# Performance work log

Measured on AMD Instinct MI355X. Metric: run time of the kernel, lower is better.

## Reference

```python
import jax, jax.numpy as jnp
import numpy as np

MODES1 = [8, 8, 12, 12]
MODES2 = [8, 8, 12, 12]
MODES3 = [8, 8, 8, 8]
LAYERS = [20, 24, 24, 32, 32]
FC_DIM = 128
IN_DIM = 5
OUT_DIM = 3
B, GX, GY, GT = 4, 128, 128, 20


def _gelu(v):
    # torch F.gelu default is the exact (erf) variant
    return jax.nn.gelu(v, approximate=False)


def _spectral_conv(x, w, m1, m2, m3):
    """x: (B,Ci,X,Y,T) float; w: (4,2,Ci,Co,m1,m2,m3) float (real/imag stacked)."""
    wc = w[:, 0] + 1j * w[:, 1]  # (4,Ci,Co,m1,m2,m3) complex64
    bs, _, X, Y, T = x.shape
    Co = wc.shape[2]
    x_ft = jnp.fft.rfftn(x, axes=(2, 3, 4))  # (B,Ci,X,Y,T//2+1) complex
    zd = min(x_ft.shape[4], m3)

    def corner(xs, ys):
        c = x_ft[:, :, xs, ys, :zd]
        # zero-pad z axis up to m3 (mirrors the zero-initialized `coeff` buffer)
        return jnp.pad(c, [(0, 0)] * 4 + [(0, m3 - zd)])

    lo1, hi1 = slice(0, m1), slice(X - m1, X)
    lo2, hi2 = slice(0, m2), slice(Y - m2, Y)
    o1 = jnp.einsum('bixyz,ioxyz->boxyz', corner(lo1, lo2), wc[0])
    o2 = jnp.einsum('bixyz,ioxyz->boxyz', corner(hi1, lo2), wc[1])
    o3 = jnp.einsum('bixyz,ioxyz->boxyz', corner(lo1, hi2), wc[2])
    o4 = jnp.einsum('bixyz,ioxyz->boxyz', corner(hi1, hi2), wc[3])

    out_ft = jnp.zeros((bs, Co, X, Y, m3), dtype=x_ft.dtype)
    out_ft = out_ft.at[:, :, :m1, :m2].set(o1)
    out_ft = out_ft.at[:, :, X - m1:, :m2].set(o2)
    out_ft = out_ft.at[:, :, :m1, Y - m2:].set(o3)
    out_ft = out_ft.at[:, :, X - m1:, Y - m2:].set(o4)
    # irfftn with s=(X,Y,T) zero-pads the truncated z axis back up, like torch
    return jnp.fft.irfftn(out_ft, s=(X, Y, T), axes=(2, 3, 4))


def setup_inputs() -> dict:
    key = jax.random.key(0)
    ks = iter(jax.random.split(key, 64))
    inp = {}
    inp['x'] = jax.random.normal(next(ks), (B, GX, GY, GT, IN_DIM), dtype=jnp.float32)
    inp['fc0_w'] = jax.random.normal(next(ks), (IN_DIM, LAYERS[0]), dtype=jnp.float32) * 0.1
    inp['fc0_b'] = jnp.zeros((LAYERS[0],), dtype=jnp.float32)
    for i in range(4):
        ci, co = LAYERS[i], LAYERS[i + 1]
        scale = 1.0 / (ci * co)
        inp[f's{i}_w'] = jax.random.uniform(
            next(ks), (4, 2, ci, co, MODES1[i], MODES2[i], MODES3[i]), dtype=jnp.float32) * scale
        inp[f'c{i}_w'] = jax.random.normal(next(ks), (co, ci), dtype=jnp.float32) * (1.0 / np.sqrt(ci))
        inp[f'c{i}_b'] = jnp.zeros((co,), dtype=jnp.float32)
    inp['fc1_w'] = jax.random.normal(next(ks), (LAYERS[-1], FC_DIM), dtype=jnp.float32) * (1.0 / np.sqrt(LAYERS[-1]))
    inp['fc1_b'] = jnp.zeros((FC_DIM,), dtype=jnp.float32)
    inp['fc2_w'] = jax.random.normal(next(ks), (FC_DIM, OUT_DIM), dtype=jnp.float32) * (1.0 / np.sqrt(FC_DIM))
    inp['fc2_b'] = jnp.zeros((OUT_DIM,), dtype=jnp.float32)
    return inp


def reference(x, fc0_w, fc0_b,
              s0_w, c0_w, c0_b,
              s1_w, c1_w, c1_b,
              s2_w, c2_w, c2_b,
              s3_w, c3_w, c3_b,
              fc1_w, fc1_b, fc2_w, fc2_b):
    h = x @ fc0_w + fc0_b                       # (B,X,Y,T,C0)
    h = jnp.transpose(h, (0, 4, 1, 2, 3))       # (B,C0,X,Y,T)
    sws = [s0_w, s1_w, s2_w, s3_w]
    cws = [c0_w, c1_w, c2_w, c3_w]
    cbs = [c0_b, c1_b, c2_b, c3_b]
    for i in range(4):
        x1 = _spectral_conv(h, sws[i], MODES1[i], MODES2[i], MODES3[i])
        x2 = jnp.einsum('bixyz,oi->boxyz', h, cws[i]) + cbs[i][None, :, None, None, None]
        h = x1 + x2
        if i != 3:
            h = _gelu(h)
    h = jnp.transpose(h, (0, 2, 3, 4, 1))       # (B,X,Y,T,C_last)
    h = _gelu(h @ fc1_w + fc1_b)
    return h @ fc2_w + fc2_b                    # (B,X,Y,T,out_dim)
```

## Files before the change

kernel.cpp:

```cpp
#include <hip/hip_runtime.h>

#define TWO_PI 6.2831853071795864769f
#define SP3 327680
#define YT 2560

static constexpr float TWC20[20]={
  1.0f, 0.9510565163f, 0.8090169944f, 0.5877852523f, 0.3090169944f,
  0.0f,-0.3090169944f,-0.5877852523f,-0.8090169944f,-0.9510565163f,
 -1.0f,-0.9510565163f,-0.8090169944f,-0.5877852523f,-0.3090169944f,
  0.0f, 0.3090169944f, 0.5877852523f, 0.8090169944f, 0.9510565163f};
static constexpr float TWS20[20]={
  0.0f, 0.3090169944f, 0.5877852523f, 0.8090169944f, 0.9510565163f,
  1.0f, 0.9510565163f, 0.8090169944f, 0.5877852523f, 0.3090169944f,
  0.0f,-0.3090169944f,-0.5877852523f,-0.8090169944f,-0.9510565163f,
 -1.0f,-0.9510565163f,-0.8090169944f,-0.5877852523f,-0.3090169944f};

static __device__ __forceinline__ float gelu_f(float u){
  float x=u*0.7071067811865475f;
  float a=fabsf(x);
  float t=__builtin_amdgcn_rcpf(fmaf(0.3275911f,a,1.0f));
  float p=fmaf(fmaf(fmaf(fmaf(1.061405429f,t,-1.453152027f),t,1.421413741f),t,
               -0.284496736f),t,0.254829592f)*t;
  float e=__expf(-a*a);
  float er=copysignf(1.0f-p*e,x);
  return 0.5f*u*(1.0f+er);
}

__global__ void k_fc0(const float* __restrict__ x, const float* __restrict__ w,
                      const float* __restrict__ bias, float* __restrict__ h){
  __shared__ float wl[100], bl[20];
  int tid=threadIdx.x;
  if(tid<100) wl[tid]=w[tid];
  if(tid<20) bl[tid]=bias[tid];
  __syncthreads();
  int p=blockIdx.x*256+tid;
  int b=p/SP3, sp=p-b*SP3;
  const float* xp=x+(long)p*5;
  float xi[5];
  #pragma unroll
  for(int i=0;i<5;i++) xi[i]=xp[i];
  float* hb=h+(long)(b*32)*SP3+sp;
  #pragma unroll
  for(int c=0;c<20;c++){
    float a=bl[c];
    #pragma unroll
    for(int i=0;i<5;i++) a+=xi[i]*wl[i*20+c];
    hb[(long)c*SP3]=a;
  }
}

template<int M2>
__global__ __launch_bounds__(512,3) void k_fwd_ty8(const float* __restrict__ h,
                                                   float* __restrict__ Fty, int Ci){
  constexpr int J=2*M2*8;
  __shared__ float2 Gc[128*33];
  __shared__ float2 tw128[128];
  int tid=threadIdx.x;
  int bid=blockIdx.x;
  int xg=bid&15, bc=bid>>4; int c=bc%Ci, b=bc/Ci;
  int x0=xg*8;
  if(tid<128){ float s,cc; sincosf(TWO_PI*tid/128.0f,&s,&cc); tw128[tid]=make_float2(cc,s); }
  __syncthreads();
  const float* hb=h+(long)(b*32+c)*SP3+x0*YT;
  float2* outp=(float2*)Fty+((long)(b*32+c)*128+x0)*J;

  for(int half=0;half<2;half++){
    if(half) __syncthreads();
    {
      int y=tid&127, xl=tid>>7;
      const float* rp=hb+(half*4+xl)*YT+y*20;
      float4 r0=*(const float4*)(rp);
      float4 r1=*(const float4*)(rp+4);
      float4 r2=*(const float4*)(rp+8);
      float4 r3=*(const float4*)(rp+12);
      float4 r4=*(const float4*)(rp+16);
      float row[20]={r0.x,r0.y,r0.z,r0.w, r1.x,r1.y,r1.z,r1.w, r2.x,r2.y,r2.z,r2.w,
                     r3.x,r3.y,r3.z,r3.w, r4.x,r4.y,r4.z,r4.w};
      float av[10],bv[10];
      #pragma unroll
      for(int t=0;t<10;t++){av[t]=row[t]+row[t+10]; bv[t]=row[t]-row[t+10];}
      float re[8],im[8];
      #pragma unroll
      for(int kz=0;kz<8;kz++){re[kz]=0.f;im[kz]=0.f;}
      #pragma unroll
      for(int t=0;t<10;t++){
        #pragma unroll
        for(int kz=0;kz<8;kz++){
          float v=(kz&1)?bv[t]:av[t];
          re[kz]+=v*TWC20[(kz*t)%20];
          im[kz]-=v*TWS20[(kz*t)%20];
        }
      }
      #pragma unroll
      for(int kz=0;kz<8;kz++) Gc[y*33+xl*8+kz]=make_float2(re[kz],im[kz]);
    }
    __syncthreads();
    for(int pi=tid;pi<2048;pi+=512){
      int y=pi>>5, col=pi&31;
      float2 a=Gc[y*33+col], bb=Gc[(y+64)*33+col];
      Gc[y*33+col]      =make_float2(a.x+bb.x, a.y+bb.y);
      Gc[(y+64)*33+col] =make_float2(a.x-bb.x, a.y-bb.y);
    }
    __syncthreads();
    for(int ip=tid;ip<(M2+1)*32;ip+=512){
      int col=ip&31, sp=ip>>5;
      int off=(sp&1)?64:0;
      float a1r=0.f,a1i=0.f,a2r=0.f,a2i=0.f;
      int jj=0;
      for(int y=0;y<64;y++){
        float2 w=tw128[jj];
        float2 d=Gc[(y+off)*33+col];
        float tr=d.x*w.x, ts=d.y*w.y, ur=d.y*w.x, us=d.x*w.y;
        a1r+=tr+ts; a1i+=ur-us;
        a2r+=tr-ts; a2i+=ur+us;
        jj=(jj+sp)&127;
      }
      int xl=col>>3, kz=col&7;
      long rowoff=(long)(half*4+xl)*J;
      if(sp<M2) outp[rowoff+sp*8+kz]=make_float2(a1r,a1i);
      if(sp>=1) outp[rowoff+(2*M2-sp)*8+kz]=make_float2(a2r,a2i);
    }
  }
}

template<int M1,int M2>
__global__ __launch_bounds__(256,3) void k_fwd_x2(const float* __restrict__ Fty,
                                                  float* __restrict__ Fm, int Ci){
  constexpr int J=2*M2*8;
  constexpr int NIT=(M1*J+255)/256;
  __shared__ float2 tile[32*J];
  __shared__ float2 tw128[128];
  int tid=threadIdx.x, bid=blockIdx.x;
  int sh=bid&1; int c=(bid>>1)%Ci; int b=bid/(2*Ci);
  if(tid<128){ float s,cc; sincosf(TWO_PI*tid/128.0f,&s,&cc); tw128[tid]=make_float2(cc,s); }
  float accr[NIT],acci[NIT];
  #pragma unroll
  for(int it=0;it<NIT;it++){accr[it]=0.f;acci[it]=0.f;}
  const float2* base=(const float2*)Fty+((long)(b*32+c)*128)*J;
  for(int xt=0;xt<4;xt++){
    __syncthreads();
    const float2* src=base+(long)xt*32*J;
    for(int idx=tid;idx<32*J;idx+=256) tile[idx]=src[idx];
    __syncthreads();
    #pragma unroll
    for(int it=0;it<NIT;it++){
      int idx=it*256+tid;
      if(idx<M1*J){
        int si=idx/J, j=idx-si*J;
        int km=(sh==0)? si : (si-M1);
        int jj=(km*(xt*32))&127;
        float ar=accr[it], ai=acci[it];
        for(int xl=0;xl<32;xl++){
          float2 w=tw128[jj];
          float2 d=tile[xl*J+j];
          ar+=d.x*w.x+d.y*w.y;
          ai+=d.y*w.x-d.x*w.y;
          jj=(jj+km)&127;
        }
        accr[it]=ar; acci[it]=ai;
      }
    }
  }
  float2* o=(float2*)Fm+(long)(b*32+c)*(2*M1)*J;
  #pragma unroll
  for(int it=0;it<NIT;it++){
    int idx=it*256+tid;
    if(idx<M1*J){
      int si=idx/J, j=idx-si*J;
      int s=sh*M1+si;
      o[(long)s*J+j]=make_float2(accr[it],acci[it]);
    }
  }
}

__global__ void k_mix(const float* __restrict__ Fm, const float* __restrict__ w,
                      float* __restrict__ Fm2, int Ci, int Co, int m1, int m2){
  int MC=m1*m2*8;
  int nch=MC/8;
  int bid=blockIdx.x;
  int chunk=bid%nch; int q=(bid/nch)&3; int b=bid/(4*nch);
  int tid=threadIdx.x;
  int M1S=2*m1, M2S=2*m2;
  int J=M2S*8;
  __shared__ float fin[32*16];
  for(int idx=tid;idx<Ci*16;idx+=blockDim.x){
    int i=idx>>4; int r=idx&15; int mll=r>>1; int ri=r&1;
    int mg=chunk*8+mll;
    int mx=mg/(m2*8); int my=(mg>>3)%m2; int kz=mg&7;
    int sx=(q&1)?(m1+mx):mx; int sy=(q&2)?(m2+my):my;
    fin[idx]=Fm[((long)((b*32+i)*M1S+sx)*J+sy*8+kz)*2+ri];
  }
  __syncthreads();
  int ml=tid&7, o=tid>>3;
  int mg=chunk*8+ml;
  int mx=mg/(m2*8); int my=(mg>>3)%m2; int kz=mg&7;
  int sx=(q&1)?(m1+mx):mx; int sy=(q&2)?(m2+my):my;
  int moff=(mx*m2+my)*8+kz;
  const float* wr=w+(long)(q*2)*Ci*Co*MC+o*MC+moff;
  const float* wi=wr+(long)Ci*Co*MC;
  long wstep=(long)Co*MC;
  float re=0.f, im=0.f;
  for(int i=0;i<Ci;i++){
    float ar=fin[i*16+ml*2], ai=fin[i*16+ml*2+1];
    float wrv=wr[i*wstep], wiv=wi[i*wstep];
    re+=ar*wrv-ai*wiv;
    im+=ar*wiv+ai*wrv;
  }
  long oidx=((long)((b*32+o)*M1S+sx)*J+sy*8+kz)*2;
  Fm2[oidx]=re; Fm2[oidx+1]=im;
}

template<int M>
__global__ __launch_bounds__(512,(M==8)?3:2) void k_inv_ytx8(const float* __restrict__ Fm2,
                                                    float* h, int Co, int do_gelu){
  constexpr int S1=2*M, S2=2*M;
  constexpr int J=S2*8;
  __shared__ __align__(16) float uni[10752];
  __shared__ __align__(16) float2 g1s[S2*66];
  __shared__ float2 tw128[128];
  int tid=threadIdx.x;
  int bid=blockIdx.x;
  int xg=bid&15, bo=bid>>4; int oc=bo%Co, b=bo/Co;
  int x0=xg*8;
  if(tid<128){ float s,cc; sincosf(TWO_PI*tid/128.0f,&s,&cc); tw128[tid]=make_float2(cc,s); }
  float2* Fm2s=(float2*)uni;
  const float2* src=(const float2*)Fm2+(long)(b*32+oc)*S1*J;
  for(int idx=tid;idx<S1*J;idx+=512) Fm2s[idx]=src[idx];
  __syncthreads();
  for(int idx=tid;idx<8*J;idx+=512){
    int xl=idx/J, j=idx-xl*J;
    int xgl=x0+xl;
    float re=0.f, im=0.f;
    int jj=0;
    for(int s=0;s<M;s++){
      float2 w=tw128[jj]; float2 d=Fm2s[s*J+j];
      re+=d.x*w.x-d.y*w.y;
      im+=d.x*w.y+d.y*w.x;
      jj=(jj+xgl)&127;
    }
    jj=((128-M)*xgl)&127;
    for(int s=M;s<S1;s++){
      float2 w=tw128[jj]; float2 d=Fm2s[s*J+j];
      re+=d.x*w.x-d.y*w.y;
      im+=d.x*w.y+d.y*w.x;
      jj=(jj+xgl)&127;
    }
    g1s[(j>>3)*66 + xl*8 + (j&7)]=make_float2(re,im);
  }
  __syncthreads();
  float* So=uni;
  const float invN=1.0f/(128.0f*128.0f*20.0f);
  float* hb=h+(long)(b*32+oc)*SP3+x0*YT;
  const float4* g4c=(const float4*)g1s;
  for(int half=0;half<2;half++){
    int y=tid&127, xlh=tid>>7;
    int xlg=half*4+xlh;
    float gyr[8],gyi[8];
    {
      int base=(xlg*8)>>1;
      #pragma unroll
      for(int q=0;q<4;q++){
        float4 d=g4c[base+q];
        gyr[2*q]=d.x;   gyi[2*q]=d.y;
        gyr[2*q+1]=d.z; gyi[2*q+1]=d.w;
      }
    }
    {
      int jm=((128-M)*y)&127;
      float ang=(float)jm*(TWO_PI/128.0f);
      float wx=__cosf(ang), wy=__sinf(ang);
      int base=(M*66+xlg*8)>>1;
      #pragma unroll
      for(int q=0;q<4;q++){
        float4 d=g4c[base+q];
        gyr[2*q]  +=d.x*wx-d.y*wy;  gyi[2*q]  +=d.x*wy+d.y*wx;
        gyr[2*q+1]+=d.z*wx-d.w*wy;  gyi[2*q+1]+=d.z*wy+d.w*wx;
      }
    }
    for(int s=1;s<M;s++){
      int jm=(s*y)&127;
      float ang=(float)jm*(TWO_PI/128.0f);
      float c=__cosf(ang), sn=__sinf(ang);
      int b1=(s*66+xlg*8)>>1, b2=((S2-s)*66+xlg*8)>>1;
      #pragma unroll
      for(int q=0;q<4;q++){
        float4 d1=g4c[b1+q], d2=g4c[b2+q];
        float Ax=d1.x+d2.x, By=d1.y-d2.y, Bx=d1.x-d2.x, Ay=d1.y+d2.y;
        gyr[2*q]  +=Ax*c-By*sn;  gyi[2*q]  +=Bx*sn+Ay*c;
        float Az=d1.z+d2.z, Bw=d1.w-d2.w, Bz=d1.z-d2.z, Aw=d1.w+d2.w;
        gyr[2*q+1]+=Az*c-Bw*sn;  gyi[2*q+1]+=Bz*sn+Aw*c;
      }
    }
    #pragma unroll
    for(int t=0;t<10;t++){
      float E=gyr[0], O=0.f;
      #pragma unroll
      for(int kz=1;kz<8;kz++){
        float term=2.0f*TWC20[(kz*t)%20]*gyr[kz]-2.0f*TWS20[(kz*t)%20]*gyi[kz];
        if(kz&1) O+=term; else E+=term;
      }
      So[tid*21+t]   =(E+O)*invN;
      So[tid*21+t+10]=(E-O)*invN;
    }
    __syncthreads();
    float* dst=hb+half*10240;
    for(int f=tid;f<10240;f+=512){
      int rr=f/20, t=f-rr*20;
      float u=dst[f]+So[rr*21+t];
      if(do_gelu) u=gelu_f(u);
      dst[f]=u;
    }
    __syncthreads();
  }
}

template<int CO>
__global__ __launch_bounds__(256,4) void k_pconv2(float* h, const float* __restrict__ w,
                                                  const float* __restrict__ bias, int Ci){
  __shared__ __align__(16) float wt[32*CO];
  __shared__ float bl[CO];
  int tid=threadIdx.x;
  for(int idx=tid;idx<Ci*CO;idx+=256){int i=idx/CO,o=idx-i*CO; wt[idx]=w[o*Ci+i];}
  if(tid<CO) bl[tid]=bias[tid];
  __syncthreads();
  long p=(long)blockIdx.x*512+tid*2;
  int b=(int)(p/SP3); int sp=(int)(p-(long)b*SP3);
  float* hb=h+(long)b*32*SP3+sp;
  float acc0[CO],acc1[CO];
  #pragma unroll
  for(int o=0;o<CO;o++){acc0[o]=bl[o];acc1[o]=bl[o];}
  for(int i=0;i<Ci;i++){
    float2 v=*(const float2*)&hb[(long)i*SP3];
    const float4* wc=(const float4*)&wt[i*CO];
    #pragma unroll
    for(int o4=0;o4<CO/4;o4++){
      float4 ww=wc[o4];
      acc0[4*o4+0]+=v.x*ww.x; acc0[4*o4+1]+=v.x*ww.y;
      acc0[4*o4+2]+=v.x*ww.z; acc0[4*o4+3]+=v.x*ww.w;
      acc1[4*o4+0]+=v.y*ww.x; acc1[4*o4+1]+=v.y*ww.y;
      acc1[4*o4+2]+=v.y*ww.z; acc1[4*o4+3]+=v.y*ww.w;
    }
  }
  #pragma unroll
  for(int o=0;o<CO;o++){
    *(float2*)&hb[(long)o*SP3]=make_float2(acc0[o],acc1[o]);
  }
}

__global__ void k_prep_w1t(const float* __restrict__ w1, float* __restrict__ w1t){
  int idx=blockIdx.x*256+threadIdx.x;
  if(idx<4096){ int jj=idx>>5, i=idx&31; w1t[idx]=w1[i*128+jj]; }
}

__global__ __launch_bounds__(256,3) void k_head_s(const float* __restrict__ h,
                       const float* __restrict__ w1t, const float* __restrict__ b1,
                       const float* __restrict__ w2, const float* __restrict__ b2,
                       float* __restrict__ out){
  long p=(long)blockIdx.x*512+threadIdx.x;
  int b=(int)(p/SP3); int sp=(int)(p-(long)b*SP3);
  const float* hb=h+(long)b*32*SP3+sp;
  float hv0[32],hv1[32];
  #pragma unroll
  for(int i=0;i<32;i++){hv0[i]=hb[(long)i*SP3]; hv1[i]=hb[(long)i*SP3+256];}
  float a00=b2[0],a01=b2[1],a02=b2[2];
  float a10=a00,a11=a01,a12=a02;
  for(int jj=0;jj<128;jj++){
    const float* wc=w1t+jj*32;
    float u0=b1[jj], u1=u0;
    #pragma unroll
    for(int q=0;q<32;q++){
      float ww=wc[q];
      u0+=hv0[q]*ww;
      u1+=hv1[q]*ww;
    }
    u0=gelu_f(u0); u1=gelu_f(u1);
    float w20=w2[jj*3], w21=w2[jj*3+1], w22=w2[jj*3+2];
    a00+=u0*w20; a01+=u0*w21; a02+=u0*w22;
    a10+=u1*w20; a11+=u1*w21; a12+=u1*w22;
  }
  float* op=out+p*3;
  op[0]=a00; op[1]=a01; op[2]=a02;
  op=out+(p+256)*3;
  op[0]=a10; op[1]=a11; op[2]=a12;
}

__global__ __launch_bounds__(256,4) void k_head2(const float* __restrict__ h,
                       const float* __restrict__ w1, const float* __restrict__ b1,
                       const float* __restrict__ w2, const float* __restrict__ b2,
                       float* __restrict__ out){
  __shared__ __align__(16) float w1t[128*32];
  __shared__ float b1l[128];
  __shared__ __align__(16) float4 w2l[128];
  __shared__ float b2l[3];
  int tid=threadIdx.x;
  for(int idx=tid;idx<4096;idx+=256){int jj=idx>>5,i=idx&31; w1t[idx]=w1[i*128+jj];}
  if(tid<128){b1l[tid]=b1[tid]; w2l[tid]=make_float4(w2[tid*3],w2[tid*3+1],w2[tid*3+2],0.f);}
  if(tid<3) b2l[tid]=b2[tid];
  __syncthreads();
  long p=(long)blockIdx.x*512+tid;
  int b=(int)(p/SP3); int sp=(int)(p-(long)b*SP3);
  const float* hb=h+(long)b*32*SP3+sp;
  float hv0[32],hv1[32];
  #pragma unroll
  for(int i=0;i<32;i++){hv0[i]=hb[(long)i*SP3]; hv1[i]=hb[(long)i*SP3+256];}
  float a00=b2l[0],a01=b2l[1],a02=b2l[2];
  float a10=a00,a11=a01,a12=a02;
  for(int jj=0;jj<128;jj++){
    const float4* wc=(const float4*)&w1t[jj*32];
    float u0=b1l[jj], u1=u0;
    #pragma unroll
    for(int q=0;q<8;q++){
      float4 ww=wc[q];
      u0+=hv0[4*q]*ww.x+hv0[4*q+1]*ww.y+hv0[4*q+2]*ww.z+hv0[4*q+3]*ww.w;
      u1+=hv1[4*q]*ww.x+hv1[4*q+1]*ww.y+hv1[4*q+2]*ww.z+hv1[4*q+3]*ww.w;
    }
    u0=gelu_f(u0); u1=gelu_f(u1);
    float4 w2v=w2l[jj];
    a00+=u0*w2v.x; a01+=u0*w2v.y; a02+=u0*w2v.z;
    a10+=u1*w2v.x; a11+=u1*w2v.y; a12+=u1*w2v.z;
  }
  float* op=out+p*3;
  op[0]=a00; op[1]=a01; op[2]=a02;
  op=out+(p+256)*3;
  op[0]=a10; op[1]=a11; op[2]=a12;
}

extern "C" void kernel_launch(void* const* d_in, const int* in_sizes, int n_in,
                              void* d_out, int out_size, void* d_ws, size_t ws_size,
                              hipStream_t stream){
  (void)in_sizes; (void)n_in; (void)out_size;
  const float* x    =(const float*)d_in[0];
  const float* fc0w =(const float*)d_in[1];
  const float* fc0b =(const float*)d_in[2];
  const float* sw[4]={(const float*)d_in[3],(const float*)d_in[6],(const float*)d_in[9],(const float*)d_in[12]};
  const float* cw[4]={(const float*)d_in[4],(const float*)d_in[7],(const float*)d_in[10],(const float*)d_in[13]};
  const float* cb[4]={(const float*)d_in[5],(const float*)d_in[8],(const float*)d_in[11],(const float*)d_in[14]};
  const float* fc1w =(const float*)d_in[15];
  const float* fc1b =(const float*)d_in[16];
  const float* fc2w =(const float*)d_in[17];
  const float* fc2b =(const float*)d_in[18];
  float* out=(float*)d_out;
  float* ws=(float*)d_ws;

  const long H_FLOATS   = 41943040L;
  const long FTY_FULL   = 6291456L;
  const long FM_FULL    = 1179648L;
  const long NEED_FULL  = H_FLOATS + FTY_FULL + 2*FM_FULL;

  float* h = ws;
  bool full = (ws_size >= (size_t)NEED_FULL*4);

  const int LAY[5]={20,24,24,32,32};
  const int M1A[4]={8,8,12,12};

  k_fc0<<<5120,256,0,stream>>>(x,fc0w,fc0b,h);

  for(int L=0;L<4;L++){
    int Ci=LAY[L], Co=LAY[L+1], m1=M1A[L], m2=M1A[L];
    int nch=m1*m2;
    long FM_B=(long)32*(2*m1)*(2*m2*8)*2;

    if(full){
      float* Fty=ws+H_FLOATS;
      float* Fm =ws+H_FLOATS+FTY_FULL;
      float* Fm2=ws+H_FLOATS+FTY_FULL+FM_FULL;
      if(m1==8)  k_fwd_ty8<8> <<<4*Ci*16,512,0,stream>>>(h,Fty,Ci);
      else       k_fwd_ty8<12><<<4*Ci*16,512,0,stream>>>(h,Fty,Ci);
      if(m1==8)  k_fwd_x2<8,8>  <<<4*Ci*2,256,0,stream>>>(Fty,Fm,Ci);
      else       k_fwd_x2<12,12><<<4*Ci*2,256,0,stream>>>(Fty,Fm,Ci);
      k_mix<<<4*4*nch,Co*8,0,stream>>>(Fm,sw[L],Fm2,Ci,Co,m1,m2);
      if(Co==24) k_pconv2<24><<<2560,256,0,stream>>>(h,cw[L],cb[L],Ci);
      else       k_pconv2<32><<<2560,256,0,stream>>>(h,cw[L],cb[L],Ci);
      if(m1==8)  k_inv_ytx8<8> <<<4*Co*16,512,0,stream>>>(Fm2,h,Co,(L!=3)?1:0);
      else       k_inv_ytx8<12><<<4*Co*16,512,0,stream>>>(Fm2,h,Co,(L!=3)?1:0);
    } else {
      float* Fty=out;
      float* Fm =out+1572864;
      float* Fm2=out+1867776;
      for(int b=0;b<4;b++){
        float* hbp=h+(long)b*32*SP3;
        if(m1==8)  k_fwd_ty8<8> <<<Ci*16,512,0,stream>>>(hbp,Fty,Ci);
        else       k_fwd_ty8<12><<<Ci*16,512,0,stream>>>(hbp,Fty,Ci);
        if(m1==8)  k_fwd_x2<8,8>  <<<Ci*2,256,0,stream>>>(Fty,Fm,Ci);
        else       k_fwd_x2<12,12><<<Ci*2,256,0,stream>>>(Fty,Fm,Ci);
        k_mix<<<4*nch,Co*8,0,stream>>>(Fm,sw[L],Fm2+b*FM_B,Ci,Co,m1,m2);
      }
      if(Co==24) k_pconv2<24><<<2560,256,0,stream>>>(h,cw[L],cb[L],Ci);
      else       k_pconv2<32><<<2560,256,0,stream>>>(h,cw[L],cb[L],Ci);
      for(int b=0;b<4;b++){
        float* hbp=h+(long)b*32*SP3;
        if(m1==8)  k_inv_ytx8<8> <<<Co*16,512,0,stream>>>(Fm2+b*FM_B,hbp,Co,(L!=3)?1:0);
        else       k_inv_ytx8<12><<<Co*16,512,0,stream>>>(Fm2+b*FM_B,hbp,Co,(L!=3)?1:0);
      }
    }
  }
  if(full){
    float* w1t=ws+H_FLOATS+FTY_FULL;
    k_prep_w1t<<<16,256,0,stream>>>(fc1w,w1t);
    k_head_s<<<2560,256,0,stream>>>(h,w1t,fc1b,fc2w,fc2b,out);
  } else {
    k_head2<<<2560,256,0,stream>>>(h,fc1w,fc1b,fc2w,fc2b,out);
  }
}
```

Baseline: 1.486 ms.

## Restructure inverse spectral kernel with y-parity split and direct float4 writes

The inverse y/t transform kernel now runs 256-thread blocks that each cover 4 x-rows instead of 8, doubling the grid. It splits the y-sum into even and odd frequency parts, so each thread produces outputs for both y and y+64 from one pass of twiddle work. Results go straight into h through float4 read-modify-write, which removes the staging shared buffer, its barriers and the shared-memory copy of Fm2 (now read from global directly). This cuts shared memory and synchronisation and halves the trig work, at the cost of more registers per thread and uncached global reads of Fm2.

```diff
diff --git a/kernel.cpp b/kernel.cpp
--- a/kernel.cpp
+++ b/kernel.cpp
@@ -211,106 +211,118 @@
 }
 
 template<int M>
-__global__ __launch_bounds__(512,(M==8)?3:2) void k_inv_ytx8(const float* __restrict__ Fm2,
+__global__ __launch_bounds__(256,4) void k_inv_ytx8(const float* __restrict__ Fm2g,
                                                     float* h, int Co, int do_gelu){
   constexpr int S1=2*M, S2=2*M;
   constexpr int J=S2*8;
-  __shared__ __align__(16) float uni[10752];
-  __shared__ __align__(16) float2 g1s[S2*66];
+  constexpr int GST=34;
+  __shared__ __align__(16) float2 g1s[S2*GST];
   __shared__ float2 tw128[128];
-  int tid=threadIdx.x;
-  int bid=blockIdx.x;
-  int xg=bid&15, bo=bid>>4; int oc=bo%Co, b=bo/Co;
-  int x0=xg*8;
+  int tid=threadIdx.x, bid=blockIdx.x;
+  int xg=bid&31, bo=bid>>5; int oc=bo%Co, b=bo/Co;
+  int x0=xg*4;
   if(tid<128){ float s,cc; sincosf(TWO_PI*tid/128.0f,&s,&cc); tw128[tid]=make_float2(cc,s); }
-  float2* Fm2s=(float2*)uni;
-  const float2* src=(const float2*)Fm2+(long)(b*32+oc)*S1*J;
-  for(int idx=tid;idx<S1*J;idx+=512) Fm2s[idx]=src[idx];
-  __syncthreads();
-  for(int idx=tid;idx<8*J;idx+=512){
+  __syncthreads();
+  const float2* Fm2=(const float2*)Fm2g+(long)(b*32+oc)*S1*J;
+  for(int idx=tid;idx<4*J;idx+=256){
     int xl=idx/J, j=idx-xl*J;
     int xgl=x0+xl;
     float re=0.f, im=0.f;
     int jj=0;
     for(int s=0;s<M;s++){
-      float2 w=tw128[jj]; float2 d=Fm2s[s*J+j];
-      re+=d.x*w.x-d.y*w.y;
-      im+=d.x*w.y+d.y*w.x;
+      float2 w=tw128[jj]; float2 d=Fm2[s*J+j];
+      re+=d.x*w.x-d.y*w.y; im+=d.x*w.y+d.y*w.x;
       jj=(jj+xgl)&127;
     }
     jj=((128-M)*xgl)&127;
     for(int s=M;s<S1;s++){
-      float2 w=tw128[jj]; float2 d=Fm2s[s*J+j];
-      re+=d.x*w.x-d.y*w.y;
-      im+=d.x*w.y+d.y*w.x;
+      float2 w=tw128[jj]; float2 d=Fm2[s*J+j];
+      re+=d.x*w.x-d.y*w.y; im+=d.x*w.y+d.y*w.x;
       jj=(jj+xgl)&127;
     }
-    g1s[(j>>3)*66 + xl*8 + (j&7)]=make_float2(re,im);
-  }
-  __syncthreads();
-  float* So=uni;
+    g1s[(j>>3)*GST + xl*8 + (j&7)]=make_float2(re,im);
+  }
+  __syncthreads();
   const float invN=1.0f/(128.0f*128.0f*20.0f);
   float* hb=h+(long)(b*32+oc)*SP3+x0*YT;
   const float4* g4c=(const float4*)g1s;
-  for(int half=0;half<2;half++){
-    int y=tid&127, xlh=tid>>7;
-    int xlg=half*4+xlh;
-    float gyr[8],gyi[8];
-    {
-      int base=(xlg*8)>>1;
-      #pragma unroll
-      for(int q=0;q<4;q++){
-        float4 d=g4c[base+q];
-        gyr[2*q]=d.x;   gyi[2*q]=d.y;
-        gyr[2*q+1]=d.z; gyi[2*q+1]=d.w;
-      }
-    }
-    {
-      int jm=((128-M)*y)&127;
-      float ang=(float)jm*(TWO_PI/128.0f);
-      float wx=__cosf(ang), wy=__sinf(ang);
-      int base=(M*66+xlg*8)>>1;
-      #pragma unroll
-      for(int q=0;q<4;q++){
-        float4 d=g4c[base+q];
-        gyr[2*q]  +=d.x*wx-d.y*wy;  gyi[2*q]  +=d.x*wy+d.y*wx;
-        gyr[2*q+1]+=d.z*wx-d.w*wy;  gyi[2*q+1]+=d.z*wy+d.w*wx;
-      }
-    }
-    for(int s=1;s<M;s++){
-      int jm=(s*y)&127;
-      float ang=(float)jm*(TWO_PI/128.0f);
-      float c=__cosf(ang), sn=__sinf(ang);
-      int b1=(s*66+xlg*8)>>1, b2=((S2-s)*66+xlg*8)>>1;
+  int y=tid&63, xl=tid>>6;
+  float Ser[8],Sei[8],Sor[8],Soi[8];
+  {
+    int base=xl*4;
+    #pragma unroll
+    for(int q=0;q<4;q++){
+      float4 d=g4c[base+q];
+      Ser[2*q]=d.x;   Sei[2*q]=d.y;
+      Ser[2*q+1]=d.z; Sei[2*q+1]=d.w;
+      Sor[2*q]=0.f;   Soi[2*q]=0.f;
+      Sor[2*q+1]=0.f; Soi[2*q+1]=0.f;
+    }
+  }
+  {
+    int jm=((128-M)*y)&127;
+    float ang=(float)jm*(TWO_PI/128.0f);
+    float wx=__cosf(ang), wy=__sinf(ang);
+    int base=M*(GST>>1)+xl*4;
+    #pragma unroll
+    for(int q=0;q<4;q++){
+      float4 d=g4c[base+q];
+      Ser[2*q]  +=d.x*wx-d.y*wy;  Sei[2*q]  +=d.x*wy+d.y*wx;
+      Ser[2*q+1]+=d.z*wx-d.w*wy;  Sei[2*q+1]+=d.z*wy+d.w*wx;
+    }
+  }
+  for(int s=1;s<M;s++){
+    int jm=(s*y)&127;
+    float ang=(float)jm*(TWO_PI/128.0f);
+    float c=__cosf(ang), sn=__sinf(ang);
+    int b1=s*(GST>>1)+xl*4, b2=(S2-s)*(GST>>1)+xl*4;
+    if(s&1){
       #pragma unroll
       for(int q=0;q<4;q++){
         float4 d1=g4c[b1+q], d2=g4c[b2+q];
         float Ax=d1.x+d2.x, By=d1.y-d2.y, Bx=d1.x-d2.x, Ay=d1.y+d2.y;
-        gyr[2*q]  +=Ax*c-By*sn;  gyi[2*q]  +=Bx*sn+Ay*c;
+        Sor[2*q]  +=Ax*c-By*sn;  Soi[2*q]  +=Bx*sn+Ay*c;
         float Az=d1.z+d2.z, Bw=d1.w-d2.w, Bz=d1.z-d2.z, Aw=d1.w+d2.w;
-        gyr[2*q+1]+=Az*c-Bw*sn;  gyi[2*q+1]+=Bz*sn+Aw*c;
-      }
-    }
+        Sor[2*q+1]+=Az*c-Bw*sn;  Soi[2*q+1]+=Bz*sn+Aw*c;
+      }
+    }else{
+      #pragma unroll
+      for(int q=0;q<4;q++){
+        float4 d1=g4c[b1+q], d2=g4c[b2+q];
+        float Ax=d1.x+d2.x, By=d1.y-d2.y, Bx=d1.x-d2.x, Ay=d1.y+d2.y;
+        Ser[2*q]  +=Ax*c-By*sn;  Sei[2*q]  +=Bx*sn+Ay*c;
+        float Az=d1.z+d2.z, Bw=d1.w-d2.w, Bz=d1.z-d2.z, Aw=d1.w+d2.w;
+        Ser[2*q+1]+=Az*c-Bw*sn;  Sei[2*q+1]+=Bz*sn+Aw*c;
+      }
+    }
+  }
+  #pragma unroll
+  for(int pm=0;pm<2;pm++){
+    float sg=pm?-1.0f:1.0f;
+    float gr[8],gi[8];
+    #pragma unroll
+    for(int k=0;k<8;k++){gr[k]=Ser[k]+sg*Sor[k]; gi[k]=Sei[k]+sg*Soi[k];}
+    float o[20];
     #pragma unroll
     for(int t=0;t<10;t++){
-      float E=gyr[0], O=0.f;
+      float E=gr[0], O=0.f;
       #pragma unroll
       for(int kz=1;kz<8;kz++){
-        float term=2.0f*TWC20[(kz*t)%20]*gyr[kz]-2.0f*TWS20[(kz*t)%20]*gyi[kz];
+        float term=2.0f*TWC20[(kz*t)%20]*gr[kz]-2.0f*TWS20[(kz*t)%20]*gi[kz];
         if(kz&1) O+=term; else E+=term;
       }
-      So[tid*21+t]   =(E+O)*invN;
-      So[tid*21+t+10]=(E-O)*invN;
-    }
-    __syncthreads();
-    float* dst=hb+half*10240;
-    for(int f=tid;f<10240;f+=512){
-      int rr=f/20, t=f-rr*20;
-      float u=dst[f]+So[rr*21+t];
-      if(do_gelu) u=gelu_f(u);
-      dst[f]=u;
-    }
-    __syncthreads();
+      o[t]=(E+O)*invN; o[t+10]=(E-O)*invN;
+    }
+    float* dp=hb+xl*YT+(y+pm*64)*20;
+    #pragma unroll
+    for(int q=0;q<5;q++){
+      float4 hv=*(const float4*)(dp+4*q);
+      float4 ov;
+      ov.x=hv.x+o[4*q];   ov.y=hv.y+o[4*q+1];
+      ov.z=hv.z+o[4*q+2]; ov.w=hv.w+o[4*q+3];
+      if(do_gelu){ov.x=gelu_f(ov.x);ov.y=gelu_f(ov.y);ov.z=gelu_f(ov.z);ov.w=gelu_f(ov.w);}
+      *(float4*)(dp+4*q)=ov;
+    }
   }
 }
 
@@ -471,8 +483,8 @@
       k_mix<<<4*4*nch,Co*8,0,stream>>>(Fm,sw[L],Fm2,Ci,Co,m1,m2);
       if(Co==24) k_pconv2<24><<<2560,256,0,stream>>>(h,cw[L],cb[L],Ci);
       else       k_pconv2<32><<<2560,256,0,stream>>>(h,cw[L],cb[L],Ci);
-      if(m1==8)  k_inv_ytx8<8> <<<4*Co*16,512,0,stream>>>(Fm2,h,Co,(L!=3)?1:0);
-      else       k_inv_ytx8<12><<<4*Co*16,512,0,stream>>>(Fm2,h,Co,(L!=3)?1:0);
+      if(m1==8)  k_inv_ytx8<8> <<<4*Co*32,256,0,stream>>>(Fm2,h,Co,(L!=3)?1:0);
+      else       k_inv_ytx8<12><<<4*Co*32,256,0,stream>>>(Fm2,h,Co,(L!=3)?1:0);
     } else {
       float* Fty=out;
       float* Fm =out+1572864;
@@ -489,8 +501,8 @@
       else       k_pconv2<32><<<2560,256,0,stream>>>(h,cw[L],cb[L],Ci);
       for(int b=0;b<4;b++){
         float* hbp=h+(long)b*32*SP3;
-        if(m1==8)  k_inv_ytx8<8> <<<Co*16,512,0,stream>>>(Fm2+b*FM_B,hbp,Co,(L!=3)?1:0);
-        else       k_inv_ytx8<12><<<Co*16,512,0,stream>>>(Fm2+b*FM_B,hbp,Co,(L!=3)?1:0);
+        if(m1==8)  k_inv_ytx8<8> <<<Co*32,256,0,stream>>>(Fm2+b*FM_B,hbp,Co,(L!=3)?1:0);
+        else       k_inv_ytx8<12><<<Co*32,256,0,stream>>>(Fm2+b*FM_B,hbp,Co,(L!=3)?1:0);
       }
     }
   }
```

New measurement: 1.694 ms. 14.0% more time.
